# Kernel tuning notes

Measured on AMD Instinct MI355X. Metric: run time of the kernel, lower is better.

## Reference

```python
import jax, jax.numpy as jnp
import numpy as np

SAMPLE_SEED = 42


def setup_inputs() -> dict:
    key = jax.random.key(0)
    B, V = 128, 128000  # batch, vocab (llama3-scale)
    k1, _ = jax.random.split(key)
    logits = jax.random.normal(k1, (B, V), dtype=jnp.float32) * 3.0
    temperature = jnp.full((1,), 0.8, dtype=jnp.float32)
    top_p = jnp.full((1,), 0.9, dtype=jnp.float32)
    return {"logits": logits, "temperature": temperature, "top_p": top_p, "top_k": 50}


def _filter_logits(logits, temperature, top_p, top_k):
    # temperature scaling
    scores = logits / temperature  # [B, V]
    # top-k: mask everything below the k-th largest score (torch.topk semantics)
    kth = jax.lax.top_k(scores, top_k)[0][:, -1:]  # [B, 1]
    scores = jnp.where(scores < kth, -jnp.inf, scores)
    # top-p (nucleus), faithful to the reference: ascending sort, remove the
    # low-probability tail whose cumulative prob <= 1 - top_p
    sorted_idx = jnp.argsort(scores, axis=-1)                      # ascending
    sorted_scores = jnp.take_along_axis(scores, sorted_idx, axis=-1)
    cumprobs = jnp.cumsum(jax.nn.softmax(sorted_scores, axis=-1), axis=-1)
    remove_sorted = cumprobs <= (1.0 - top_p)                      # [B, V] bool
    inv_perm = jnp.argsort(sorted_idx, axis=-1)                    # invert the sort permutation
    remove = jnp.take_along_axis(remove_sorted, inv_perm, axis=-1)
    return jnp.where(remove, -jnp.inf, scores)


def reference(logits, temperature, top_p, top_k):
    filtered = _filter_logits(logits, temperature, top_p, top_k)   # [B, V]
    probs = jax.nn.softmax(filtered, axis=-1)                      # torch.softmax(...)
    # multinomial(probs, 1) == categorical over the filtered logits
    next_token = jax.random.categorical(jax.random.key(SAMPLE_SEED), filtered, axis=-1)
    return next_token.astype(jnp.int32), probs
```

## Files before the change

### kernel.cpp

```cpp
#include <hip/hip_runtime.h>
#include <stdint.h>

#define VOCAB     128000
#define BINS      4096
#define BPR       2
#define CHUNK     (VOCAB / BPR)
#define N4C       (CHUNK / 4)
#define NSAMP4    (N4C / 8)
#define TILES     16
#define TILE4     (VOCAB / 4 / TILES)
#define TPBF      256
#define STCAP     1536
#define CAND_CAP  3072
#define FILT_CAP  512
#define KEEP_CAP  128

typedef float nfloat4 __attribute__((ext_vector_type(4)));

__device__ __forceinline__ uint32_t rotl32(uint32_t x, uint32_t r) {
    return (x << r) | (x >> (32u - r));
}

__device__ __forceinline__ uint32_t f2ord(float f) {
    uint32_t u = __float_as_uint(f);
    return (u & 0x80000000u) ? ~u : (u | 0x80000000u);
}

__device__ __forceinline__ void threefry_0_42(uint32_t x0, uint32_t x1,
                                              uint32_t& o0, uint32_t& o1) {
    const uint32_t k0 = 0u, k1 = 42u;
    const uint32_t k2 = 0x1BD11BDAu ^ k0 ^ k1;
#define TF_RND(R) { x0 += x1; x1 = rotl32(x1, (R)); x1 ^= x0; }
    x0 += k0; x1 += k1;
    TF_RND(13) TF_RND(15) TF_RND(26) TF_RND(6)
    x0 += k1; x1 += k2 + 1u;
    TF_RND(17) TF_RND(29) TF_RND(16) TF_RND(24)
    x0 += k2; x1 += k0 + 2u;
    TF_RND(13) TF_RND(15) TF_RND(26) TF_RND(6)
    x0 += k0; x1 += k1 + 3u;
    TF_RND(17) TF_RND(29) TF_RND(16) TF_RND(24)
    x0 += k1; x1 += k2 + 4u;
    TF_RND(13) TF_RND(15) TF_RND(26) TF_RND(6)
    x0 += k2; x1 += k0 + 5u;
#undef TF_RND
    o0 = x0; o1 = x1;
}

__device__ __forceinline__ float gumbel_at(uint64_t flat) {
    uint32_t o0, o1;
    threefry_0_42((uint32_t)(flat >> 32), (uint32_t)flat, o0, o1);
    uint32_t bits = o0 ^ o1;
    float f = __uint_as_float((bits >> 9) | 0x3F800000u) - 1.0f;
    float u = (f == 0.0f) ? 1.17549435e-38f : f;
    return -logf(-logf(u));
}

extern "C" __global__ __launch_bounds__(1024)
void hist_kernel(const float* __restrict__ logits,
                 const float* __restrict__ temp_p,
                 const int*   __restrict__ topk_p,
                 int* __restrict__ tbins,
                 int* __restrict__ counters,
                 int batch) {
    const int row = blockIdx.x / BPR;
    const int sub = blockIdx.x % BPR;
    const int c0  = sub * CHUNK;
    const int tid = threadIdx.x;

    const float rT = 1.0f / temp_p[0];
    const int   K  = topk_p[0];

    __shared__ int hist[BINS];
    __shared__ int s_grp[256];

    for (int i = tid; i < BINS; i += 1024) hist[i] = 0;
    __syncthreads();

    const float4* rowp = (const float4*)(logits + (size_t)row * VOCAB) + (c0 >> 2);

    for (int s = tid; s < NSAMP4; s += 1024) {
        int i4 = ((s >> 2) << 5) + (s & 3);
        float4 v = rowp[i4];
        atomicAdd(&hist[f2ord(v.x * rT) >> 20], 1);
        atomicAdd(&hist[f2ord(v.y * rT) >> 20], 1);
        atomicAdd(&hist[f2ord(v.z * rT) >> 20], 1);
        atomicAdd(&hist[f2ord(v.w * rT) >> 20], 1);
    }
    __syncthreads();

    if (tid < 256) {
        int s = 0;
        #pragma unroll
        for (int b = 0; b < 16; ++b) s += hist[tid * 16 + b];
        s_grp[tid] = s;
    }
    __syncthreads();
    if (tid == 0) {
        int cum = 0, g = 255;
        for (; g > 0; --g) {
            if (cum + s_grp[g] >= K) break;
            cum += s_grp[g];
        }
        int tb = g * 16;
        for (int b = g * 16 + 15; ; --b) {
            cum += hist[b];
            if (cum >= K || b == g * 16) { tb = b; break; }
        }
        tbins[row * BPR + sub] = tb;
        if (sub == 0) counters[row] = 0;
    }
}

extern "C" __global__ __launch_bounds__(TPBF)
void filter_kernel(const float* __restrict__ logits,
                   const float* __restrict__ temp_p,
                   const int*   __restrict__ tbins,
                   float* __restrict__ out,
                   float* __restrict__ candV,
                   int*   __restrict__ candI,
                   int*   __restrict__ counters,
                   int batch, int cap) {
    const int bid = blockIdx.x;
    const int row = bid / TILES;
    const int t   = bid % TILES;
    const int tid = threadIdx.x;
    const int base4 = t * TILE4;

    __shared__ float stV[STCAP];
    __shared__ int   stI[STCAP];
    __shared__ int   s_cnt;
    __shared__ int   s_base;

    if (tid == 0) s_cnt = 0;
    __syncthreads();

    const float rT = 1.0f / temp_p[0];
    const uint32_t tbin = (uint32_t)tbins[row * BPR + (t >> 3)];

    const float4* rowp = (const float4*)(logits + (size_t)row * VOCAB) + base4;
    float4*       orow = (float4*)(out + batch + (size_t)row * VOCAB) + base4;
    const nfloat4 z4 = { 0.0f, 0.0f, 0.0f, 0.0f };

    int* ctr = &counters[row];
    float* cVrow = candV + (size_t)row * cap;
    int*   cIrow = candI + (size_t)row * cap;

    #pragma unroll
    for (int u = 0; u < 8; ++u) {
        int i = u * TPBF + tid;
        if (i < TILE4) {
            float4 v = rowp[i];
            float ss[4] = { v.x * rT, v.y * rT, v.z * rT, v.w * rT };
            int e = (base4 + i) * 4;
            #pragma unroll
            for (int c = 0; c < 4; ++c) {
                if ((f2ord(ss[c]) >> 20) >= tbin) {
                    int p = atomicAdd(&s_cnt, 1);
                    if (p < STCAP) { stV[p] = ss[c]; stI[p] = e + c; }
                    else {
                        int q = atomicAdd(ctr, 1);
                        if (q < cap) { cVrow[q] = ss[c]; cIrow[q] = e + c; }
                    }
                }
            }
            __builtin_nontemporal_store(z4, (nfloat4*)&orow[i]);
        }
    }
    __syncthreads();

    const int staged = min(s_cnt, STCAP);
    if (tid == 0) s_base = atomicAdd(ctr, staged);
    __syncthreads();
    const int base = s_base;
    for (int i = tid; i < staged; i += TPBF) {
        int dst = base + i;
        if (dst < cap) { cVrow[dst] = stV[i]; cIrow[dst] = stI[i]; }
    }
}

extern "C" __global__ __launch_bounds__(512)
void finalize_kernel(const float* __restrict__ topp_p,
                     const int*   __restrict__ topk_p,
                     const float* __restrict__ candV,
                     const int*   __restrict__ candI,
                     const int*   __restrict__ counters,
                     float* __restrict__ out,
                     int batch, int cap) {
    const int row  = blockIdx.x;
    const int tid  = threadIdx.x;
    const int nthr = blockDim.x;

    const float thresh = 1.0f - topp_p[0];
    const int   K      = topk_p[0];

    __shared__ float    cV[CAND_CAP];
    __shared__ int      cI[CAND_CAP];
    __shared__ uint32_t h2[BINS];
    __shared__ int      s_grp[256];
    __shared__ float    fV[FILT_CAP];
    __shared__ int      fI[FILT_CAP];
    __shared__ float    sV[FILT_CAP];
    __shared__ int      sI[FILT_CAP];
    __shared__ float    eArr[KEEP_CAP * 2];
    __shared__ float    s_gs[KEEP_CAP];
    __shared__ int      s_bstar, s_cnt2, s_Kp, s_M, s_token;
    __shared__ float    s_Z2;

    const int n = min(counters[row], cap);
    const float* cVrow = candV + (size_t)row * cap;
    const int*   cIrow = candI + (size_t)row * cap;
    for (int i = tid; i < n; i += nthr) { cV[i] = cVrow[i]; cI[i] = cIrow[i]; }
    for (int i = tid; i < BINS; i += nthr) h2[i] = 0u;
    if (tid == 0) s_cnt2 = 0;
    __syncthreads();

    for (int i = tid; i < n; i += nthr) atomicAdd(&h2[f2ord(cV[i]) >> 20], 1u);
    __syncthreads();
    if (tid < 256) {
        int s = 0;
        #pragma unroll
        for (int b = 0; b < 16; ++b) s += (int)h2[tid * 16 + b];
        s_grp[tid] = s;
    }
    __syncthreads();
    if (tid == 0) {
        int cum = 0, g = 255;
        for (; g > 0; --g) {
            if (cum + s_grp[g] >= K) break;
            cum += s_grp[g];
        }
        int tb = g * 16;
        for (int b = g * 16 + 15; ; --b) {
            cum += (int)h2[b];
            if (cum >= K || b == g * 16) { tb = b; break; }
        }
        s_bstar = tb;
    }
    __syncthreads();
    const uint32_t bstar = (uint32_t)s_bstar;

    for (int i = tid; i < n; i += nthr) {
        if ((f2ord(cV[i]) >> 20) >= bstar) {
            int p = atomicAdd(&s_cnt2, 1);
            if (p < FILT_CAP) { fV[p] = cV[i]; fI[p] = cI[i]; }
        }
    }
    __syncthreads();
    const int n2 = min(s_cnt2, FILT_CAP);

    for (int j = tid; j < n2; j += nthr) {
        float vj = fV[j]; int ij = fI[j];
        int r = 0;
        for (int l = 0; l < n2; ++l) {
            float vl = fV[l];
            r += (vl > vj) || (vl == vj && fI[l] < ij);
        }
        sV[r] = vj; sI[r] = ij;
    }
    __syncthreads();

    if (tid == 0) {
        int Keff = min(K, n2);
        float kth = sV[Keff - 1];
        int Kp = Keff;
        while (Kp < n2 && sV[Kp] == kth) ++Kp;
        if (Kp > KEEP_CAP * 2) Kp = KEEP_CAP * 2;
        s_Kp = Kp;
    }
    __syncthreads();
    const int Kp = s_Kp;
    const float m = sV[0];
    for (int j = tid; j < Kp; j += nthr) eArr[j] = expf(sV[j] - m);
    __syncthreads();

    if (tid == 0) {
        float Z = 0.0f;
        for (int j = Kp - 1; j >= 0; --j) Z += eArr[j];
        float cum = 0.0f; int jcut = 0;
        for (int j = Kp - 1; j >= 0; --j) {
            cum += eArr[j] / Z;
            if (cum > thresh) { jcut = j; break; }
        }
        int M = jcut + 1;
        if (M > KEEP_CAP) M = KEEP_CAP;
        float Z2 = 0.0f;
        for (int j = 0; j < M; ++j) Z2 += eArr[j];
        s_M = M; s_Z2 = Z2;
    }
    __syncthreads();
    const int M = s_M;
    const float Z2 = s_Z2;

    if (tid < M) {
        uint64_t flat = (uint64_t)row * VOCAB + (uint32_t)sI[tid];
        s_gs[tid] = sV[tid] + gumbel_at(flat);
    }
    __syncthreads();
    if (tid == 0) {
        float bs = -__builtin_inff(); int bi = 0x7fffffff;
        for (int j = 0; j < M; ++j) {
            float s = s_gs[j]; int c = sI[j];
            if (s > bs || (s == bs && c < bi)) { bs = s; bi = c; }
        }
        s_token = bi;
    }
    __syncthreads();

    for (int j = tid; j < M; j += nthr) {
        out[batch + (size_t)row * VOCAB + sI[j]] = eArr[j] / Z2;
    }
    if (tid == 0) out[row] = (float)s_token;
}

extern "C" void kernel_launch(void* const* d_in, const int* in_sizes, int n_in,
                              void* d_out, int out_size, void* d_ws, size_t ws_size,
                              hipStream_t stream) {
    (void)n_in; (void)out_size;
    const float* logits = (const float*)d_in[0];
    const float* temp   = (const float*)d_in[1];
    const float* topp   = (const float*)d_in[2];
    const int*   topk   = (const int*)d_in[3];
    float* out = (float*)d_out;

    const int batch = in_sizes[0] / VOCAB;

    size_t hdr_bytes = ((size_t)batch * 3 * sizeof(int) + 255) & ~(size_t)255;
    int cap = CAND_CAP;
    if (ws_size > hdr_bytes) {
        size_t per_row = (ws_size - hdr_bytes) / ((size_t)batch * 8);
        if (per_row < (size_t)cap) cap = (int)per_row;
    }
    int*   counters = (int*)d_ws;
    int*   tbins    = counters + batch;
    float* candV    = (float*)((char*)d_ws + hdr_bytes);
    int*   candI    = (int*)(candV + (size_t)batch * cap);

    hist_kernel<<<batch * BPR, 1024, 0, stream>>>(
        logits, temp, topk, tbins, counters, batch);

    filter_kernel<<<batch * TILES, TPBF, 0, stream>>>(
        logits, temp, tbins, out, candV, candI, counters, batch, cap);

    finalize_kernel<<<batch, 512, 0, stream>>>(
        topp, topk, candV, candI, counters, out, batch, cap);
}
```

Baseline: 56.47 us.

## Fuse per-row histogram threshold estimation into filter kernel, drop hist kernel

Removes the separate histogram kernel. Each filter block now builds its own coarse 2048-bin histogram from a small sample of its tile and picks a local top-k threshold bin, which saves one launch and one extra read pass. Because the sample is per tile and coarser, more candidates pass the filter, so the candidate capacity is raised to 16384. The finalize kernel now reads candidates directly from global memory instead of staging them in shared memory. Counters are zeroed with a memset, and the main load is hoisted ahead of the bounds check.

```diff
diff --git a/kernel.cpp b/kernel.cpp
--- a/kernel.cpp
+++ b/kernel.cpp
@@ -2,17 +2,15 @@
 #include <stdint.h>
 
 #define VOCAB     128000
+#define HBINS     2048
 #define BINS      4096
-#define BPR       2
-#define CHUNK     (VOCAB / BPR)
-#define N4C       (CHUNK / 4)
-#define NSAMP4    (N4C / 8)
 #define TILES     16
 #define TILE4     (VOCAB / 4 / TILES)
+#define NS4       252
 #define TPBF      256
-#define STCAP     1536
-#define CAND_CAP  3072
-#define FILT_CAP  512
+#define STCAP     1024
+#define CAND_CAP  16384
+#define FILT_CAP  1024
 #define KEEP_CAP  128
 
 typedef float nfloat4 __attribute__((ext_vector_type(4)));
@@ -55,66 +53,10 @@
     return -logf(-logf(u));
 }
 
-extern "C" __global__ __launch_bounds__(1024)
-void hist_kernel(const float* __restrict__ logits,
-                 const float* __restrict__ temp_p,
-                 const int*   __restrict__ topk_p,
-                 int* __restrict__ tbins,
-                 int* __restrict__ counters,
-                 int batch) {
-    const int row = blockIdx.x / BPR;
-    const int sub = blockIdx.x % BPR;
-    const int c0  = sub * CHUNK;
-    const int tid = threadIdx.x;
-
-    const float rT = 1.0f / temp_p[0];
-    const int   K  = topk_p[0];
-
-    __shared__ int hist[BINS];
-    __shared__ int s_grp[256];
-
-    for (int i = tid; i < BINS; i += 1024) hist[i] = 0;
-    __syncthreads();
-
-    const float4* rowp = (const float4*)(logits + (size_t)row * VOCAB) + (c0 >> 2);
-
-    for (int s = tid; s < NSAMP4; s += 1024) {
-        int i4 = ((s >> 2) << 5) + (s & 3);
-        float4 v = rowp[i4];
-        atomicAdd(&hist[f2ord(v.x * rT) >> 20], 1);
-        atomicAdd(&hist[f2ord(v.y * rT) >> 20], 1);
-        atomicAdd(&hist[f2ord(v.z * rT) >> 20], 1);
-        atomicAdd(&hist[f2ord(v.w * rT) >> 20], 1);
-    }
-    __syncthreads();
-
-    if (tid < 256) {
-        int s = 0;
-        #pragma unroll
-        for (int b = 0; b < 16; ++b) s += hist[tid * 16 + b];
-        s_grp[tid] = s;
-    }
-    __syncthreads();
-    if (tid == 0) {
-        int cum = 0, g = 255;
-        for (; g > 0; --g) {
-            if (cum + s_grp[g] >= K) break;
-            cum += s_grp[g];
-        }
-        int tb = g * 16;
-        for (int b = g * 16 + 15; ; --b) {
-            cum += hist[b];
-            if (cum >= K || b == g * 16) { tb = b; break; }
-        }
-        tbins[row * BPR + sub] = tb;
-        if (sub == 0) counters[row] = 0;
-    }
-}
-
 extern "C" __global__ __launch_bounds__(TPBF)
 void filter_kernel(const float* __restrict__ logits,
                    const float* __restrict__ temp_p,
-                   const int*   __restrict__ tbins,
+                   const int*   __restrict__ topk_p,
                    float* __restrict__ out,
                    float* __restrict__ candV,
                    int*   __restrict__ candI,
@@ -126,21 +68,57 @@
     const int tid = threadIdx.x;
     const int base4 = t * TILE4;
 
+    __shared__ int   hist[HBINS];
+    __shared__ int   s_grp[256];
     __shared__ float stV[STCAP];
     __shared__ int   stI[STCAP];
-    __shared__ int   s_cnt;
-    __shared__ int   s_base;
-
+    __shared__ int   s_tbin, s_cnt, s_base;
+
+    #pragma unroll
+    for (int i = tid; i < HBINS; i += TPBF) hist[i] = 0;
     if (tid == 0) s_cnt = 0;
     __syncthreads();
 
     const float rT = 1.0f / temp_p[0];
-    const uint32_t tbin = (uint32_t)tbins[row * BPR + (t >> 3)];
+    const int   K  = topk_p[0];
 
     const float4* rowp = (const float4*)(logits + (size_t)row * VOCAB) + base4;
     float4*       orow = (float4*)(out + batch + (size_t)row * VOCAB) + base4;
     const nfloat4 z4 = { 0.0f, 0.0f, 0.0f, 0.0f };
 
+    if (tid < NS4) {
+        int i4 = ((tid >> 2) << 5) + (tid & 3);
+        float4 v = rowp[i4];
+        atomicAdd(&hist[f2ord(v.x * rT) >> 21], 1);
+        atomicAdd(&hist[f2ord(v.y * rT) >> 21], 1);
+        atomicAdd(&hist[f2ord(v.z * rT) >> 21], 1);
+        atomicAdd(&hist[f2ord(v.w * rT) >> 21], 1);
+    }
+    __syncthreads();
+
+    {
+        int s = 0;
+        #pragma unroll
+        for (int b = 0; b < 8; ++b) s += hist[tid * 8 + b];
+        s_grp[tid] = s;
+    }
+    __syncthreads();
+    if (tid == 0) {
+        int cum = 0, g = 255;
+        for (; g > 0; --g) {
+            if (cum + s_grp[g] >= K) break;
+            cum += s_grp[g];
+        }
+        int tb = g * 8;
+        for (int b = g * 8 + 7; ; --b) {
+            cum += hist[b];
+            if (cum >= K || b == g * 8) { tb = b; break; }
+        }
+        s_tbin = tb;
+    }
+    __syncthreads();
+    const uint32_t tbin = (uint32_t)s_tbin;
+
     int* ctr = &counters[row];
     float* cVrow = candV + (size_t)row * cap;
     int*   cIrow = candI + (size_t)row * cap;
@@ -148,13 +126,14 @@
     #pragma unroll
     for (int u = 0; u < 8; ++u) {
         int i = u * TPBF + tid;
+        int ic = i < TILE4 ? i : TILE4 - 1;
+        float4 v = rowp[ic];
         if (i < TILE4) {
-            float4 v = rowp[i];
             float ss[4] = { v.x * rT, v.y * rT, v.z * rT, v.w * rT };
             int e = (base4 + i) * 4;
             #pragma unroll
             for (int c = 0; c < 4; ++c) {
-                if ((f2ord(ss[c]) >> 20) >= tbin) {
+                if ((f2ord(ss[c]) >> 21) >= tbin) {
                     int p = atomicAdd(&s_cnt, 1);
                     if (p < STCAP) { stV[p] = ss[c]; stI[p] = e + c; }
                     else {
@@ -193,8 +172,6 @@
     const float thresh = 1.0f - topp_p[0];
     const int   K      = topk_p[0];
 
-    __shared__ float    cV[CAND_CAP];
-    __shared__ int      cI[CAND_CAP];
     __shared__ uint32_t h2[BINS];
     __shared__ int      s_grp[256];
     __shared__ float    fV[FILT_CAP];
@@ -209,12 +186,11 @@
     const int n = min(counters[row], cap);
     const float* cVrow = candV + (size_t)row * cap;
     const int*   cIrow = candI + (size_t)row * cap;
-    for (int i = tid; i < n; i += nthr) { cV[i] = cVrow[i]; cI[i] = cIrow[i]; }
     for (int i = tid; i < BINS; i += nthr) h2[i] = 0u;
     if (tid == 0) s_cnt2 = 0;
     __syncthreads();
 
-    for (int i = tid; i < n; i += nthr) atomicAdd(&h2[f2ord(cV[i]) >> 20], 1u);
+    for (int i = tid; i < n; i += nthr) atomicAdd(&h2[f2ord(cVrow[i]) >> 20], 1u);
     __syncthreads();
     if (tid < 256) {
         int s = 0;
@@ -240,9 +216,10 @@
     const uint32_t bstar = (uint32_t)s_bstar;
 
     for (int i = tid; i < n; i += nthr) {
-        if ((f2ord(cV[i]) >> 20) >= bstar) {
+        float v = cVrow[i];
+        if ((f2ord(v) >> 20) >= bstar) {
             int p = atomicAdd(&s_cnt2, 1);
-            if (p < FILT_CAP) { fV[p] = cV[i]; fI[p] = cI[i]; }
+            if (p < FILT_CAP) { fV[p] = v; fI[p] = cIrow[i]; }
         }
     }
     __syncthreads();
@@ -324,22 +301,20 @@
 
     const int batch = in_sizes[0] / VOCAB;
 
-    size_t hdr_bytes = ((size_t)batch * 3 * sizeof(int) + 255) & ~(size_t)255;
+    size_t hdr_bytes = ((size_t)batch * sizeof(int) + 255) & ~(size_t)255;
     int cap = CAND_CAP;
     if (ws_size > hdr_bytes) {
         size_t per_row = (ws_size - hdr_bytes) / ((size_t)batch * 8);
         if (per_row < (size_t)cap) cap = (int)per_row;
     }
     int*   counters = (int*)d_ws;
-    int*   tbins    = counters + batch;
     float* candV    = (float*)((char*)d_ws + hdr_bytes);
     int*   candI    = (int*)(candV + (size_t)batch * cap);
 
-    hist_kernel<<<batch * BPR, 1024, 0, stream>>>(
-        logits, temp, topk, tbins, counters, batch);
+    hipMemsetAsync(counters, 0, (size_t)batch * sizeof(int), stream);
 
     filter_kernel<<<batch * TILES, TPBF, 0, stream>>>(
-        logits, temp, tbins, out, candV, candI, counters, batch, cap);
+        logits, temp, topk, out, candV, candI, counters, batch, cap);
 
     finalize_kernel<<<batch, 512, 0, stream>>>(
         topp, topk, candV, candI, counters, out, batch, cap);
```

Measured after the change: 62.00 us. 9.8% more time.
